# Kernel tuning notes

Hardware: AMD Instinct MI355X
Metric: run time of the kernel (lower is better)

## Reference

```python
import jax, jax.numpy as jnp
import numpy as np

B, H, W, C = 2, 64, 64, 256
NH, K = 8, 7  # num_heads, neighborhood kernel size


def setup_inputs() -> dict:
    key = jax.random.key(0)
    ks = jax.random.split(key, 8)
    xav = lambda k, shape: jax.random.normal(k, shape, jnp.float32) * np.sqrt(2.0 / (shape[0] + shape[1])).astype(np.float32)
    return {
        "x": jax.random.normal(ks[0], (B, H, W, C), jnp.float32),
        "norm1_g": jnp.ones((C,), jnp.float32),
        "norm1_b": jnp.zeros((C,), jnp.float32),
        "qkv_w": xav(ks[1], (3 * C, C)),
        "qkv_b": jnp.zeros((3 * C,), jnp.float32),
        "rpb": jax.random.normal(ks[2], (NH, 2 * K - 1, 2 * K - 1), jnp.float32) * 0.02,
        "proj_w": xav(ks[3], (C, C)),
        "proj_b": jnp.zeros((C,), jnp.float32),
        "norm2_g": jnp.ones((C,), jnp.float32),
        "norm2_b": jnp.zeros((C,), jnp.float32),
        "fc1_w": xav(ks[4], (4 * C, C)),
        "fc1_b": jnp.zeros((4 * C,), jnp.float32),
        "fc2_w": xav(ks[5], (C, 4 * C)),
        "fc2_b": jnp.zeros((C,), jnp.float32),
    }


def _layernorm(x, g, b, eps=1e-5):
    m = x.mean(-1, keepdims=True)
    v = jnp.mean((x - m) ** 2, axis=-1, keepdims=True)
    return (x - m) * jax.lax.rsqrt(v + eps) * g + b


def _nat2d(x, qkv_w, qkv_b, rpb, proj_w, proj_b):
    """Neighborhood attention 2D (NATTEN semantics: edge-clamped k x k windows,
    relative positional bias indexed by key_pos - query_pos + k - 1)."""
    b, h, w, c = x.shape
    nh = rpb.shape[0]
    k = (rpb.shape[1] + 1) // 2
    dh = c // nh
    qkv = (x @ qkv_w.T + qkv_b).reshape(b, h, w, 3, nh, dh)
    q = qkv[..., 0, :, :] * (dh ** -0.5)  # [b,h,w,nh,dh]
    kk = qkv[..., 1, :, :]
    vv = qkv[..., 2, :, :]
    # edge-clamped window starts per query row/col
    starts_h = jnp.clip(jnp.arange(h) - k // 2, 0, h - k)
    starts_w = jnp.clip(jnp.arange(w) - k // 2, 0, w - k)
    idx_h = starts_h[:, None] + jnp.arange(k)  # [h,k] key row indices
    idx_w = starts_w[:, None] + jnp.arange(k)  # [w,k] key col indices
    # gather neighborhoods -> [b,h,w,k,k,nh,dh]
    knb = kk[:, idx_h][:, :, :, idx_w].transpose(0, 1, 3, 2, 4, 5, 6)
    vnb = vv[:, idx_h][:, :, :, idx_w].transpose(0, 1, 3, 2, 4, 5, 6)
    attn = jnp.einsum('bijhd,bijklhd->bijhkl', q, knb)  # [b,h,w,nh,k,k]
    # relative positional bias: index = key - query + (k-1) in [0, 2k-2]
    rb_h = idx_h - jnp.arange(h)[:, None] + (k - 1)  # [h,k]
    rb_w = idx_w - jnp.arange(w)[:, None] + (k - 1)  # [w,k]
    bias = rpb[:, rb_h][:, :, :, rb_w]  # [nh,h,k,w,k]
    bias = bias.transpose(1, 3, 0, 2, 4)  # [h,w,nh,k,k]
    attn = jax.nn.softmax((attn + bias).reshape(b, h, w, nh, k * k), axis=-1)
    out = jnp.einsum('bijhn,bijnhd->bijhd', attn, vnb.reshape(b, h, w, k * k, nh, dh))
    return out.reshape(b, h, w, c) @ proj_w.T + proj_b


def reference(x, norm1_g, norm1_b, qkv_w, qkv_b, rpb, proj_w, proj_b,
              norm2_g, norm2_b, fc1_w, fc1_b, fc2_w, fc2_b):
    # norm -> neighborhood attention -> residual
    x = x + _nat2d(_layernorm(x, norm1_g, norm1_b), qkv_w, qkv_b, rpb, proj_w, proj_b)
    # norm -> MLP (gelu) -> residual
    hdn = _layernorm(x, norm2_g, norm2_b)
    hdn = jax.nn.gelu(hdn @ fc1_w.T + fc1_b, approximate=False)
    return x + (hdn @ fc2_w.T + fc2_b)
```

## Files before the change

kernel.cpp:

```cpp
#include <hip/hip_runtime.h>

typedef __attribute__((ext_vector_type(8))) short bf16x8;
typedef __attribute__((ext_vector_type(4))) float f32x4;
typedef unsigned short u16;

__device__ __forceinline__ float bf2f(u16 u) {
    return __builtin_bit_cast(float, ((unsigned int)u) << 16);
}
__device__ __forceinline__ u16 f2bf(float f) {
    unsigned int x = __builtin_bit_cast(unsigned int, f);
    x += 0x7FFFu + ((x >> 16) & 1u);
    return (u16)(x >> 16);
}
__device__ __forceinline__ int swz(int row) { return (row ^ (row >> 2)) & 3; }

typedef const __attribute__((address_space(1))) void* gas_t;
typedef __attribute__((address_space(3))) void* las_t;
__device__ __forceinline__ void load_lds16(const u16* g, u16* l) {
    __builtin_amdgcn_global_load_lds((gas_t)g, (las_t)l, 16, 0, 0);
}

__global__ __launch_bounds__(256) void prep_kernel(
    const float* __restrict__ x, const float* __restrict__ g, const float* __restrict__ b,
    const float* __restrict__ s0, const float* __restrict__ s1,
    const float* __restrict__ s2, const float* __restrict__ s3,
    u16* __restrict__ wbf, u16* __restrict__ y)
{
    const int bid = blockIdx.x, tid = threadIdx.x;
    {
        int idx = bid * 256 + tid;
        #pragma unroll
        for (int r = 0; r < 2; ++r) {
            if (r == 1) {
                if (tid >= 128) break;
                idx = 524288 + bid * 128 + tid;
            }
            const float* src; int off;
            if      (idx < 196608) { src = s0; off = idx; }
            else if (idx < 262144) { src = s1; off = idx - 196608; }
            else if (idx < 524288) { src = s2; off = idx - 262144; }
            else                   { src = s3; off = idx - 524288; }
            wbf[idx] = f2bf(src[off]);
        }
    }
    const int tok  = bid * 4 + (tid >> 6);
    const int lane = tid & 63;
    float4 v = *(const float4*)(x + (size_t)tok * 256 + lane * 4);
    float s  = v.x + v.y + v.z + v.w;
    float sq = v.x*v.x + v.y*v.y + v.z*v.z + v.w*v.w;
    #pragma unroll
    for (int off = 32; off; off >>= 1) {
        s  += __shfl_xor(s, off);
        sq += __shfl_xor(sq, off);
    }
    const float mean = s * (1.0f / 256.0f);
    const float var  = sq * (1.0f / 256.0f) - mean * mean;
    const float rs   = rsqrtf(var + 1e-5f);
    float4 gv = *(const float4*)(g + lane * 4);
    float4 bv = *(const float4*)(b + lane * 4);
    ushort4 o;
    o.x = f2bf((v.x - mean) * rs * gv.x + bv.x);
    o.y = f2bf((v.y - mean) * rs * gv.y + bv.y);
    o.z = f2bf((v.z - mean) * rs * gv.z + bv.z);
    o.w = f2bf((v.w - mean) * rs * gv.w + bv.w);
    *(ushort4*)(y + (size_t)tok * 256 + lane * 4) = o;
}

template<int BN, int N, int K, int EPI>
__global__ __launch_bounds__(256) void gemm_m97(
    const u16* __restrict__ A, const u16* __restrict__ W,
    const float* __restrict__ bias, const float* __restrict__ res,
    void* __restrict__ outv)
{
    constexpr int MT = (BN == 128) ? 4 : 2;
    constexpr int NT = 4;
    __shared__ u16 As[128 * 32];
    __shared__ u16 Bs[BN * 32];
    const int tid  = threadIdx.x;
    const int lane = tid & 63;
    const int wave = tid >> 6;
    const int m0   = blockIdx.x * 128;
    const int n0   = blockIdx.y * BN;
    const int wm0  = (BN == 128) ? (wave >> 1) * 64 : wave * 32;
    const int wn0  = (BN == 128) ? (wave & 1) * 64 : 0;

    f32x4 acc[MT][NT];
    #pragma unroll
    for (int mt = 0; mt < MT; ++mt)
        #pragma unroll
        for (int nt = 0; nt < NT; ++nt)
            acc[mt][nt] = (f32x4){0.f, 0.f, 0.f, 0.f};

    int aoff[2], boff[BN / 64];
    #pragma unroll
    for (int r = 0; r < 2; ++r) {
        const int s   = r * 256 + tid;
        const int row = s >> 2;
        aoff[r] = row * K + ((s & 3) ^ swz(row)) * 8;
    }
    #pragma unroll
    for (int r = 0; r < BN / 64; ++r) {
        const int s   = r * 256 + tid;
        const int row = s >> 2;
        boff[r] = row * K + ((s & 3) ^ swz(row)) * 8;
    }
    const int fr = lane & 15;
    const int lc = lane >> 4;

    for (int k0 = 0; k0 < K; k0 += 32) {
        __syncthreads();
        #pragma unroll
        for (int r = 0; r < 2; ++r)
            load_lds16(A + (size_t)m0 * K + k0 + aoff[r], As + (r * 256 + tid) * 8);
        #pragma unroll
        for (int r = 0; r < BN / 64; ++r)
            load_lds16(W + (size_t)n0 * K + k0 + boff[r], Bs + (r * 256 + tid) * 8);
        __syncthreads();
        bf16x8 af[MT], bw[NT];
        #pragma unroll
        for (int mt = 0; mt < MT; ++mt) {
            const int rr = wm0 + mt * 16 + fr;
            af[mt] = *(const bf16x8*)(As + rr * 32 + (lc ^ swz(rr)) * 8);
        }
        #pragma unroll
        for (int nt = 0; nt < NT; ++nt) {
            const int rr = wn0 + nt * 16 + fr;
            bw[nt] = *(const bf16x8*)(Bs + rr * 32 + (lc ^ swz(rr)) * 8);
        }
        #pragma unroll
        for (int mt = 0; mt < MT; ++mt)
            #pragma unroll
            for (int nt = 0; nt < NT; ++nt)
                acc[mt][nt] = __builtin_amdgcn_mfma_f32_16x16x32_bf16(af[mt], bw[nt], acc[mt][nt], 0, 0, 0);
    }

    const int col = lane & 15;
    const int rb  = (lane >> 4) * 4;
    #pragma unroll
    for (int nt = 0; nt < NT; ++nt) {
        const int n  = n0 + wn0 + nt * 16 + col;
        const float bv = bias[n];
        #pragma unroll
        for (int mt = 0; mt < MT; ++mt) {
            #pragma unroll
            for (int r = 0; r < 4; ++r) {
                const int m = m0 + wm0 + mt * 16 + rb + r;
                float v = acc[mt][nt][r] + bv;
                if (EPI == 1) {
                    if (n < 256) v *= 0.1767766952966369f;
                    ((u16*)outv)[(size_t)m * N + n] = f2bf(v);
                }
                if (EPI == 2) {
                    v += res[(size_t)m * N + n];
                    ((float*)outv)[(size_t)m * N + n] = v;
                }
                if (EPI == 3) {
                    v = 0.5f * v * (1.0f + erff(v * 0.7071067811865475f));
                    ((u16*)outv)[(size_t)m * N + n] = f2bf(v);
                }
            }
        }
    }
}

__global__ __launch_bounds__(256) void proj_ln_kernel(
    const u16* __restrict__ A, const u16* __restrict__ W, const float* __restrict__ pb,
    const float* __restrict__ xres, const float* __restrict__ g2, const float* __restrict__ b2,
    float* __restrict__ x1, u16* __restrict__ ln2out)
{
    __shared__ u16 As[64 * 32];
    __shared__ u16 Bs[256 * 32];
    const int tid  = threadIdx.x;
    const int lane = tid & 63;
    const int wave = tid >> 6;
    const int m0   = blockIdx.x * 64;

    f32x4 acc[16];
    #pragma unroll
    for (int nt = 0; nt < 16; ++nt) acc[nt] = (f32x4){0.f, 0.f, 0.f, 0.f};

    const int arow = tid >> 2, acs = tid & 3;
    const int aoff = (m0 + arow) * 256 + (acs ^ (arow & 3)) * 8;
    int boff[4];
    #pragma unroll
    for (int r = 0; r < 4; ++r) {
        const int s   = r * 256 + tid;
        const int row = s >> 2;
        boff[r] = row * 256 + ((s & 3) ^ (row & 3)) * 8;
    }
    const int fr = lane & 15;
    const int fc = lane >> 4;

    for (int k0 = 0; k0 < 256; k0 += 32) {
        __syncthreads();
        load_lds16(A + aoff + k0, As + tid * 8);
        #pragma unroll
        for (int r = 0; r < 4; ++r)
            load_lds16(W + boff[r] + k0, Bs + (r * 256 + tid) * 8);
        __syncthreads();
        const int ra = wave * 16 + fr;
        bf16x8 af = *(const bf16x8*)(As + ra * 32 + (fc ^ (ra & 3)) * 8);
        #pragma unroll
        for (int nt = 0; nt < 16; ++nt) {
            const int rbq = nt * 16 + fr;
            bf16x8 bw = *(const bf16x8*)(Bs + rbq * 32 + (fc ^ (rbq & 3)) * 8);
            acc[nt] = __builtin_amdgcn_mfma_f32_16x16x32_bf16(af, bw, acc[nt], 0, 0, 0);
        }
    }

    const int col = lane & 15;
    const int g   = lane >> 4;
    float s[4] = {0.f, 0.f, 0.f, 0.f}, sq[4] = {0.f, 0.f, 0.f, 0.f};
    #pragma unroll
    for (int nt = 0; nt < 16; ++nt) {
        const int n = nt * 16 + col;
        const float bv = pb[n];
        #pragma unroll
        for (int r = 0; r < 4; ++r) {
            const int m = m0 + wave * 16 + g * 4 + r;
            float v = acc[nt][r] + bv + xres[(size_t)m * 256 + n];
            acc[nt][r] = v;
            s[r] += v; sq[r] += v * v;
        }
    }
    #pragma unroll
    for (int off = 1; off < 16; off <<= 1) {
        #pragma unroll
        for (int r = 0; r < 4; ++r) {
            s[r]  += __shfl_xor(s[r], off);
            sq[r] += __shfl_xor(sq[r], off);
        }
    }
    float mean[4], rs[4];
    #pragma unroll
    for (int r = 0; r < 4; ++r) {
        mean[r] = s[r] * (1.0f / 256.0f);
        const float var = sq[r] * (1.0f / 256.0f) - mean[r] * mean[r];
        rs[r] = rsqrtf(var + 1e-5f);
    }
    #pragma unroll
    for (int nt = 0; nt < 16; ++nt) {
        const int n = nt * 16 + col;
        const float gam = g2[n], bet = b2[n];
        #pragma unroll
        for (int r = 0; r < 4; ++r) {
            const int m = m0 + wave * 16 + g * 4 + r;
            const float v = acc[nt][r];
            x1[(size_t)m * 256 + n] = v;
            ln2out[(size_t)m * 256 + n] = f2bf((v - mean[r]) * rs[r] * gam + bet);
        }
    }
}

__global__ __launch_bounds__(256, 2) void attn_tile_kernel(
    const u16* __restrict__ qkv, const float* __restrict__ rpb,
    u16* __restrict__ out)
{
    __shared__ u16   kv[100 * 64];
    __shared__ u16   qs[16 * 32];
    __shared__ float probs[16 * 66];

    const int tid  = threadIdx.x;
    const int bb   = blockIdx.x >> 8;
    const int rem  = blockIdx.x & 255;
    const int ti0  = (rem >> 4) << 2;
    const int tj0  = (rem & 15) << 2;
    const int oh   = min(max(ti0 - 3, 0), 54);
    const int ow   = min(max(tj0 - 3, 0), 54);
    const int tokbase = bb * 4096;

    int off_kv[4];
    #pragma unroll
    for (int r = 0; r < 4; ++r) {
        const int s  = r * 256 + tid;
        const int t  = s >> 3;
        const int c  = (s & 7) ^ (t & 7);
        const int tr = t / 10, tc = t - tr * 10;
        const int tokg = tokbase + (oh + tr) * 64 + (ow + tc);
        off_kv[r] = tokg * 768 + 256 + ((c & 4) << 6) + (c & 3) * 8;
    }
    const int tq   = tid >> 2;
    const int qoff = (tokbase + (ti0 + (tq >> 2)) * 64 + (tj0 + (tq & 3))) * 768
                   + (tid & 3) * 8;

    const int token = tid >> 4;
    const int part  = tid & 15;
    const int li = token >> 2, lj = token & 3;
    const int i  = ti0 + li,   j  = tj0 + lj;
    const int sh = min(max(i - 3, 0), 57);
    const int sw = min(max(j - 3, 0), 57);
    const int rowbase  = (sh - oh) * 10 + (sw - ow);
    const int rb_const = (sh - i + 6) * 13 + (sw - j + 6);
    const size_t outbase = (size_t)(tokbase + i * 64 + j) * 256 + part * 2;

    for (int h = 0; h < 8; ++h) {
        __syncthreads();
        const int hoff = h * 32;
        #pragma unroll
        for (int r = 0; r < 3; ++r)
            load_lds16(qkv + off_kv[r] + hoff, kv + (r * 256 + tid) * 8);
        if (tid < 32)
            load_lds16(qkv + off_kv[3] + hoff, kv + (768 + tid) * 8);
        if (tid < 64)
            load_lds16(qkv + qoff + hoff, qs + tid * 8);
        __syncthreads();

        float qv[32];
        #pragma unroll
        for (int c = 0; c < 4; ++c) {
            bf16x8 v = *(const bf16x8*)(qs + token * 32 + c * 8);
            #pragma unroll
            for (int e = 0; e < 8; ++e) qv[c * 8 + e] = bf2f((u16)v[e]);
        }

        float sc[4];
        #pragma unroll
        for (int sidx = 0; sidx < 4; ++sidx) {
            const int n = part + sidx * 16;
            if (n < 49) {
                const int kh = n / 7, kw = n - (n / 7) * 7;
                const int hidx = rowbase + kh * 10 + kw;
                float acc = rpb[h * 169 + rb_const + kh * 13 + kw];
                #pragma unroll
                for (int c = 0; c < 4; ++c) {
                    const int slot = (hidx << 3) + (c ^ (hidx & 7));
                    bf16x8 kk = *(const bf16x8*)(kv + slot * 8);
                    #pragma unroll
                    for (int e = 0; e < 8; ++e)
                        acc += qv[c * 8 + e] * bf2f((u16)kk[e]);
                }
                sc[sidx] = acc;
            } else {
                sc[sidx] = -1e30f;
            }
        }
        float mx = fmaxf(fmaxf(sc[0], sc[1]), fmaxf(sc[2], sc[3]));
        #pragma unroll
        for (int off = 1; off < 16; off <<= 1) mx = fmaxf(mx, __shfl_xor(mx, off));
        float ex[4], ssum = 0.f;
        #pragma unroll
        for (int sidx = 0; sidx < 4; ++sidx) {
            ex[sidx] = __expf(sc[sidx] - mx);
            ssum += ex[sidx];
        }
        #pragma unroll
        for (int off = 1; off < 16; off <<= 1) ssum += __shfl_xor(ssum, off);
        const float inv = 1.0f / ssum;
        #pragma unroll
        for (int sidx = 0; sidx < 4; ++sidx)
            probs[token * 66 + part + sidx * 16] = ex[sidx] * inv;
        __syncthreads();

        float o0 = 0.f, o1 = 0.f;
        const int vchunk = 4 + (part >> 2);
        const int vsub   = (part & 3) * 2;
        #pragma unroll
        for (int kh = 0; kh < 7; ++kh) {
            #pragma unroll
            for (int kw = 0; kw < 7; ++kw) {
                const int n    = kh * 7 + kw;
                const int hidx = rowbase + kh * 10 + kw;
                const float p  = probs[token * 66 + n];
                const int slot = (hidx << 3) + (vchunk ^ (hidx & 7));
                const unsigned int vv = *(const unsigned int*)(kv + slot * 8 + vsub);
                o0 += p * bf2f((u16)(vv & 0xffffu));
                o1 += p * bf2f((u16)(vv >> 16));
            }
        }
        ushort2 ov;
        ov.x = f2bf(o0); ov.y = f2bf(o1);
        *(ushort2*)(out + outbase + hoff) = ov;
    }
}

extern "C" void kernel_launch(void* const* d_in, const int* in_sizes, int n_in,
                              void* d_out, int out_size, void* d_ws, size_t ws_size,
                              hipStream_t stream)
{
    const float* x      = (const float*)d_in[0];
    const float* n1g    = (const float*)d_in[1];
    const float* n1b    = (const float*)d_in[2];
    const float* qkv_w  = (const float*)d_in[3];
    const float* qkv_b  = (const float*)d_in[4];
    const float* rpb    = (const float*)d_in[5];
    const float* proj_w = (const float*)d_in[6];
    const float* proj_b = (const float*)d_in[7];
    const float* n2g    = (const float*)d_in[8];
    const float* n2b    = (const float*)d_in[9];
    const float* fc1_w  = (const float*)d_in[10];
    const float* fc1_b  = (const float*)d_in[11];
    const float* fc2_w  = (const float*)d_in[12];
    const float* fc2_b  = (const float*)d_in[13];
    float* out = (float*)d_out;

    char* wsb = (char*)d_ws;
    u16*   wbf   = (u16*)wsb;
    u16*   qkvW  = wbf;
    u16*   projW = wbf + 196608;
    u16*   fc1W  = wbf + 262144;
    u16*   fc2W  = wbf + 524288;
    u16*   ln1   = (u16*)(wsb + 1572864);
    u16*   attnB = ln1;
    u16*   qkvB  = (u16*)(wsb + 5767168);
    u16*   ln2   = qkvB;
    u16*   hbuf  = (u16*)(wsb + 9961472);
    float* x1    = (float*)(wsb + 26738688);

    dim3 blk(256);
    prep_kernel<<<2048, blk, 0, stream>>>(x, n1g, n1b, qkv_w, proj_w, fc1_w, fc2_w, wbf, ln1);
    gemm_m97<128, 768, 256, 1><<<dim3(64, 6), blk, 0, stream>>>(ln1, qkvW, qkv_b, nullptr, qkvB);
    attn_tile_kernel<<<512, blk, 0, stream>>>(qkvB, rpb, attnB);
    proj_ln_kernel<<<128, blk, 0, stream>>>(attnB, projW, proj_b, x, n2g, n2b, x1, ln2);
    gemm_m97<128, 1024, 256, 3><<<dim3(64, 8), blk, 0, stream>>>(ln2, fc1W, fc1_b, nullptr, hbuf);
    gemm_m97<64, 256, 1024, 2><<<dim3(64, 4), blk, 0, stream>>>(hbuf, fc2W, fc2_b, x1, out);
}
```

Baseline: 173.9 us.

## Use 128x64 GEMM tiles with K=64 stages and 8-way LDS swizzle

Replaces the templated GEMM (128x128 or 128x64 tiles, K step 32) with a single 128x64 tile kernel that loads K=64 per stage and uses an 8-chunk XOR swizzle in LDS. The QKV and FC1 GEMMs now launch twice as many blocks, which spreads them over more CUs and halves the number of barrier-separated k iterations. In exchange each block reuses less data per tile, so more A-matrix traffic goes to global memory, and LDS use per block goes up.

```diff
diff --git a/kernel.cpp b/kernel.cpp
--- a/kernel.cpp
+++ b/kernel.cpp
@@ -12,7 +12,6 @@
     x += 0x7FFFu + ((x >> 16) & 1u);
     return (u16)(x >> 16);
 }
-__device__ __forceinline__ int swz(int row) { return (row ^ (row >> 2)) & 3; }
 
 typedef const __attribute__((address_space(1))) void* gas_t;
 typedef __attribute__((address_space(3))) void* las_t;
@@ -66,82 +65,82 @@
     *(ushort4*)(y + (size_t)tok * 256 + lane * 4) = o;
 }
 
-template<int BN, int N, int K, int EPI>
-__global__ __launch_bounds__(256) void gemm_m97(
+template<int N, int K, int EPI>
+__global__ __launch_bounds__(256) void gemm128x64(
     const u16* __restrict__ A, const u16* __restrict__ W,
     const float* __restrict__ bias, const float* __restrict__ res,
     void* __restrict__ outv)
 {
-    constexpr int MT = (BN == 128) ? 4 : 2;
-    constexpr int NT = 4;
-    __shared__ u16 As[128 * 32];
-    __shared__ u16 Bs[BN * 32];
+    __shared__ u16 As[128 * 64];
+    __shared__ u16 Bs[64 * 64];
     const int tid  = threadIdx.x;
     const int lane = tid & 63;
     const int wave = tid >> 6;
     const int m0   = blockIdx.x * 128;
-    const int n0   = blockIdx.y * BN;
-    const int wm0  = (BN == 128) ? (wave >> 1) * 64 : wave * 32;
-    const int wn0  = (BN == 128) ? (wave & 1) * 64 : 0;
-
-    f32x4 acc[MT][NT];
-    #pragma unroll
-    for (int mt = 0; mt < MT; ++mt)
-        #pragma unroll
-        for (int nt = 0; nt < NT; ++nt)
+    const int n0   = blockIdx.y * 64;
+    const int wm0  = wave * 32;
+
+    f32x4 acc[2][4];
+    #pragma unroll
+    for (int mt = 0; mt < 2; ++mt)
+        #pragma unroll
+        for (int nt = 0; nt < 4; ++nt)
             acc[mt][nt] = (f32x4){0.f, 0.f, 0.f, 0.f};
 
-    int aoff[2], boff[BN / 64];
+    int aoff[4], boff[2];
+    #pragma unroll
+    for (int r = 0; r < 4; ++r) {
+        const int s   = r * 256 + tid;
+        const int row = s >> 3;
+        aoff[r] = row * K + ((s & 7) ^ (row & 7)) * 8;
+    }
     #pragma unroll
     for (int r = 0; r < 2; ++r) {
         const int s   = r * 256 + tid;
-        const int row = s >> 2;
-        aoff[r] = row * K + ((s & 3) ^ swz(row)) * 8;
-    }
-    #pragma unroll
-    for (int r = 0; r < BN / 64; ++r) {
-        const int s   = r * 256 + tid;
-        const int row = s >> 2;
-        boff[r] = row * K + ((s & 3) ^ swz(row)) * 8;
+        const int row = s >> 3;
+        boff[r] = row * K + ((s & 7) ^ (row & 7)) * 8;
     }
     const int fr = lane & 15;
     const int lc = lane >> 4;
 
-    for (int k0 = 0; k0 < K; k0 += 32) {
-        __syncthreads();
+    for (int k0 = 0; k0 < K; k0 += 64) {
+        __syncthreads();
+        #pragma unroll
+        for (int r = 0; r < 4; ++r)
+            load_lds16(A + (size_t)m0 * K + k0 + aoff[r], As + (r * 256 + tid) * 8);
         #pragma unroll
         for (int r = 0; r < 2; ++r)
-            load_lds16(A + (size_t)m0 * K + k0 + aoff[r], As + (r * 256 + tid) * 8);
-        #pragma unroll
-        for (int r = 0; r < BN / 64; ++r)
             load_lds16(W + (size_t)n0 * K + k0 + boff[r], Bs + (r * 256 + tid) * 8);
         __syncthreads();
-        bf16x8 af[MT], bw[NT];
-        #pragma unroll
-        for (int mt = 0; mt < MT; ++mt) {
-            const int rr = wm0 + mt * 16 + fr;
-            af[mt] = *(const bf16x8*)(As + rr * 32 + (lc ^ swz(rr)) * 8);
-        }
-        #pragma unroll
-        for (int nt = 0; nt < NT; ++nt) {
-            const int rr = wn0 + nt * 16 + fr;
-            bw[nt] = *(const bf16x8*)(Bs + rr * 32 + (lc ^ swz(rr)) * 8);
-        }
-        #pragma unroll
-        for (int mt = 0; mt < MT; ++mt)
-            #pragma unroll
-            for (int nt = 0; nt < NT; ++nt)
-                acc[mt][nt] = __builtin_amdgcn_mfma_f32_16x16x32_bf16(af[mt], bw[nt], acc[mt][nt], 0, 0, 0);
+        #pragma unroll
+        for (int ks = 0; ks < 2; ++ks) {
+            bf16x8 af[2], bw[4];
+            #pragma unroll
+            for (int mt = 0; mt < 2; ++mt) {
+                const int rr = wm0 + mt * 16 + fr;
+                af[mt] = *(const bf16x8*)(As + rr * 64 + ((ks * 4 + lc) ^ (rr & 7)) * 8);
+            }
+            #pragma unroll
+            for (int nt = 0; nt < 4; ++nt) {
+                const int rr = nt * 16 + fr;
+                bw[nt] = *(const bf16x8*)(Bs + rr * 64 + ((ks * 4 + lc) ^ (rr & 7)) * 8);
+            }
+            #pragma unroll
+            for (int mt = 0; mt < 2; ++mt)
+                #pragma unroll
+                for (int nt = 0; nt < 4; ++nt)
+                    acc[mt][nt] = __builtin_amdgcn_mfma_f32_16x16x32_bf16(af[mt], bw[nt], acc[mt][nt], 0, 0, 0);
+        }
     }
 
     const int col = lane & 15;
     const int rb  = (lane >> 4) * 4;
     #pragma unroll
-    for (int nt = 0; nt < NT; ++nt) {
-        const int n  = n0 + wn0 + nt * 16 + col;
+    for (int nt = 0; nt < 4; ++nt) {
+        const int n  = n0 + nt * 16 + col;
         const float bv = bias[n];
         #pragma unroll
-        for (int mt = 0; mt < MT; ++mt) {
+        for (int mt = 0; mt < 2; ++mt) {
             #pragma unroll
             for (int r = 0; r < 4; ++r) {
                 const int m = m0 + wm0 + mt * 16 + rb + r;
@@ -408,9 +407,9 @@
 
     dim3 blk(256);
     prep_kernel<<<2048, blk, 0, stream>>>(x, n1g, n1b, qkv_w, proj_w, fc1_w, fc2_w, wbf, ln1);
-    gemm_m97<128, 768, 256, 1><<<dim3(64, 6), blk, 0, stream>>>(ln1, qkvW, qkv_b, nullptr, qkvB);
+    gemm128x64<768, 256, 1><<<dim3(64, 12), blk, 0, stream>>>(ln1, qkvW, qkv_b, nullptr, qkvB);
     attn_tile_kernel<<<512, blk, 0, stream>>>(qkvB, rpb, attnB);
     proj_ln_kernel<<<128, blk, 0, stream>>>(attnB, projW, proj_b, x, n2g, n2b, x1, ln2);
-    gemm_m97<128, 1024, 256, 3><<<dim3(64, 8), blk, 0, stream>>>(ln2, fc1W, fc1_b, nullptr, hbuf);
-    gemm_m97<64, 256, 1024, 2><<<dim3(64, 4), blk, 0, stream>>>(hbuf, fc2W, fc2_b, x1, out);
-}
+    gemm128x64<1024, 256, 3><<<dim3(64, 16), blk, 0, stream>>>(ln2, fc1W, fc1_b, nullptr, hbuf);
+    gemm128x64<256, 1024, 2><<<dim3(64, 4), blk, 0, stream>>>(hbuf, fc2W, fc2_b, x1, out);
+}
```

Result: faster. 165.9 us (-4.6%).
